# Performance work log

Measured on AMD Instinct MI355X. Metric: run time of the kernel, lower is better.

The kernel has to match this reference:

```python
import jax, jax.numpy as jnp
import numpy as np

ALPHA = 0.2          # LeakyReLU negative slope
NEG_INF = -9e15      # mask value used by the original module


def setup_inputs() -> dict:
    key = jax.random.key(0)
    k1, k2, k3, k4 = jax.random.split(key, 4)
    N, F_IN, F_OUT = 8192, 512, 256
    inp = jax.random.normal(k1, (N, F_IN), dtype=jnp.float32)
    W = jax.random.normal(k2, (F_IN, F_OUT), dtype=jnp.float32) * (1.414 / np.sqrt(F_IN))
    a = jax.random.normal(k3, (2 * F_OUT, 1), dtype=jnp.float32) * (1.414 / np.sqrt(F_OUT))
    adj = jax.random.randint(k4, (N, N), 0, 2, dtype=jnp.int32)
    return {"input": inp, "W": W, "a": a, "adj": adj}


def reference(input, W, a, adj):
    # h: [N, F_out]
    h = input @ W
    F_out = h.shape[1]
    # Original builds a_input[i,j] = concat(h_i, h_j) then matmuls with a.
    # Equivalent: e_ij = leakyrelu(h_i . a[:F] + h_j . a[F:]) without the O(N^2 * 2F) tensor.
    a1 = a[:F_out, 0]   # [F_out]
    a2 = a[F_out:, 0]   # [F_out]
    s1 = h @ a1         # [N]
    s2 = h @ a2         # [N]
    e = jax.nn.leaky_relu(s1[:, None] + s2[None, :], negative_slope=ALPHA)  # [N, N]
    attention = jax.nn.softmax(jnp.where(adj > 0, e, NEG_INF), axis=1)       # [N, N]
    return attention @ h  # [N, F_out]
```

## Files before the change

### kernel.cpp

```cpp
#include <hip/hip_runtime.h>


typedef __attribute__((ext_vector_type(8))) short bf16x8;
typedef __attribute__((ext_vector_type(4))) float fx4;
typedef __attribute__((ext_vector_type(4))) int ix4;
typedef __attribute__((ext_vector_type(2))) unsigned int ux2;

#define NN 8192
#define FIN 512
#define FOUT 256
#define PS 136
#define AROWS 32

__device__ __forceinline__ unsigned short f2bf(float f) {
    unsigned int x = __float_as_uint(f);
    x += 0x7fffu + ((x >> 16) & 1u);
    return (unsigned short)(x >> 16);
}
__device__ __forceinline__ bf16x8 pack8(fx4 a, fx4 b) {
    bf16x8 r;
    r[0] = (short)f2bf(a[0]); r[1] = (short)f2bf(a[1]);
    r[2] = (short)f2bf(a[2]); r[3] = (short)f2bf(a[3]);
    r[4] = (short)f2bf(b[0]); r[5] = (short)f2bf(b[1]);
    r[6] = (short)f2bf(b[2]); r[7] = (short)f2bf(b[3]);
    return r;
}

__global__ void wt_kernel(const float* __restrict__ W,
                          unsigned short* __restrict__ WTt) {
    const int c = threadIdx.x;
    const int k = blockIdx.x;
    WTt[((size_t)(k >> 5) * 256 + c) * 32 + (k & 31)] = f2bf(W[k * FOUT + c]);
}

__global__ __launch_bounds__(256) void prep_kernel(
    const float* __restrict__ X,
    const unsigned short* __restrict__ WTt,
    const float* __restrict__ A,
    const int* __restrict__ adj,
    unsigned short* __restrict__ hTt,
    float* __restrict__ s1, float* __restrict__ s2,
    unsigned int* __restrict__ mask)
{
    __shared__ float s1sh[4][16], s2sh[4][16];
    const int tid = threadIdx.x;

    if (blockIdx.x >= 512) {
        const int g = (blockIdx.x - 512) * 256 + tid;
        const int* base = adj + (size_t)g * 32;
        ix4 v[8];
#pragma unroll
        for (int k = 0; k < 8; ++k) v[k] = *(const ix4*)(base + k * 4);
        unsigned int m = 0;
#pragma unroll
        for (int k = 0; k < 8; ++k)
#pragma unroll
            for (int j = 0; j < 4; ++j)
                m |= (v[k][j] != 0 ? 1u : 0u) << (k * 4 + j);
        mask[g] = m;
        return;
    }

    const int w = tid >> 6, l = tid & 63, q = l >> 4, lr = l & 15;
    const int r0 = blockIdx.x * 16;
    const int cbase = w * 64;
    fx4 acc[4] = {};

    for (int kb = 0; kb < FIN; kb += 32) {
        const float* xp = X + (size_t)(r0 + lr) * FIN + kb + q * 8;
        bf16x8 a0 = pack8(*(const fx4*)xp, *(const fx4*)(xp + 4));
#pragma unroll
        for (int tc = 0; tc < 4; ++tc) {
            bf16x8 b = *(const bf16x8*)(WTt + ((size_t)(kb >> 5) * 256 + cbase + tc * 16 + lr) * 32 + q * 8);
            acc[tc] = __builtin_amdgcn_mfma_f32_16x16x32_bf16(a0, b, acc[tc], 0, 0, 0);
        }
    }

    const int jb = r0 >> 5, jo = (r0 & 31) + q * 4;
#pragma unroll
    for (int tc = 0; tc < 4; ++tc) {
        const int c = cbase + tc * 16 + lr;
        ux2 hp;
        hp.x = (unsigned)f2bf(acc[tc][0]) | ((unsigned)f2bf(acc[tc][1]) << 16);
        hp.y = (unsigned)f2bf(acc[tc][2]) | ((unsigned)f2bf(acc[tc][3]) << 16);
        *(ux2*)(hTt + ((size_t)jb * 256 + c) * 32 + jo) = hp;
    }

    float p1[4] = {}, p2[4] = {};
#pragma unroll
    for (int tc = 0; tc < 4; ++tc) {
        const int c = cbase + tc * 16 + lr;
        const float a1v = A[c], a2v = A[FOUT + c];
#pragma unroll
        for (int r = 0; r < 4; ++r) {
            p1[r] += acc[tc][r] * a1v;
            p2[r] += acc[tc][r] * a2v;
        }
    }
#pragma unroll
    for (int r = 0; r < 4; ++r) {
#pragma unroll
        for (int off = 1; off < 16; off <<= 1) {
            p1[r] += __shfl_xor(p1[r], off);
            p2[r] += __shfl_xor(p2[r], off);
        }
        if (lr == 0) { s1sh[w][q * 4 + r] = p1[r]; s2sh[w][q * 4 + r] = p2[r]; }
    }
    __syncthreads();
    if (tid < 16) {
        s1[r0 + tid] = s1sh[0][tid] + s1sh[1][tid] + s1sh[2][tid] + s1sh[3][tid];
        s2[r0 + tid] = s2sh[0][tid] + s2sh[1][tid] + s2sh[2][tid] + s2sh[3][tid];
    }
}

__global__ __launch_bounds__(512) void attn_kernel(
    const unsigned int* __restrict__ mask,
    const unsigned short* __restrict__ hTt,
    const float* __restrict__ s1,
    const float* __restrict__ s2,
    float* __restrict__ out)
{
    __shared__ unsigned short P[2][AROWS * PS];
    __shared__ float dsh[AROWS];

    const int tid = threadIdx.x;
    const int r0 = blockIdx.x * AROWS;

    const int prow = tid >> 4;
    const int pq = tid & 15;
    const float s1v = s1[r0 + prow];
    const unsigned int* mrow = mask + (size_t)(r0 + prow) * 256;
    const int mshift = (pq & 3) * 8;
    float denp = 0.f;

    const int w = tid >> 6, l = tid & 63, q = l >> 4, lr = l & 15;
    const int cbase = w * 32;
    fx4 acc[2][2] = {};

    struct LSet { unsigned int mval; fx4 s2a, s2b; };
    LSet LA, LB;
    bf16x8 B0[4][2], B1[4][2];

    auto loadP = [&](int kt, LSet& L) {
        L.mval = mrow[kt * 4 + (pq >> 2)];
        L.s2a = *(const fx4*)(s2 + kt * 128 + pq * 8);
        L.s2b = *(const fx4*)(s2 + kt * 128 + pq * 8 + 4);
    };
    auto calcP = [&](int b, const LSet& L) {
        const unsigned int mbyte = (L.mval >> mshift) & 0xFFu;
        bf16x8 pv;
#pragma unroll
        for (int j = 0; j < 8; ++j) {
            const float s2j = (j < 4) ? L.s2a[j] : L.s2b[j - 4];
            float t = s1v + s2j;
            float e = fmaxf(t, 0.2f * t);
            e = fminf(e, 30.f);
            const float p = ((mbyte >> j) & 1u) ? __expf(e) : 0.f;
            denp += p;
            pv[j] = (short)f2bf(p);
        }
        *(bf16x8*)(&P[b][prow * PS + pq * 8]) = pv;
    };
    auto loadB = [&](int it, bf16x8 (&B)[4][2]) {
#pragma unroll
        for (int ks = 0; ks < 4; ++ks)
#pragma unroll
            for (int tc = 0; tc < 2; ++tc)
                B[ks][tc] = *(const bf16x8*)(hTt + ((size_t)(it * 4 + ks) * 256 + cbase + tc * 16 + lr) * 32 + q * 8);
    };

    auto ldsBarrier = [&]() {
        asm volatile("s_waitcnt lgkmcnt(0)" ::: "memory");
        __builtin_amdgcn_s_barrier();
    };

    const int ITERS = NN / 128;
    loadP(0, LA);
    calcP(0, LA);
    loadP(1, LA);
    loadB(0, B0);
    ldsBarrier();

    auto body = [&](int it, bf16x8 (&Bc)[4][2], bf16x8 (&Bn)[4][2],
                    LSet& Lc, LSet& Ln) {
        if (it + 1 < ITERS) loadB(it + 1, Bn);
        if (it + 2 < ITERS) loadP(it + 2, Ln);
        const unsigned short* Pb = P[it & 1];
        bf16x8 af0[4], af1[4];
#pragma unroll
        for (int ks = 0; ks < 4; ++ks) {
            af0[ks] = *(const bf16x8*)(Pb + lr * PS + ks * 32 + q * 8);
            af1[ks] = *(const bf16x8*)(Pb + (16 + lr) * PS + ks * 32 + q * 8);
        }
        __builtin_amdgcn_s_setprio(1);
#pragma unroll
        for (int ks = 0; ks < 4; ++ks)
#pragma unroll
            for (int tc = 0; tc < 2; ++tc) {
                acc[0][tc] = __builtin_amdgcn_mfma_f32_16x16x32_bf16(af0[ks], Bc[ks][tc], acc[0][tc], 0, 0, 0);
                acc[1][tc] = __builtin_amdgcn_mfma_f32_16x16x32_bf16(af1[ks], Bc[ks][tc], acc[1][tc], 0, 0, 0);
            }
        __builtin_amdgcn_s_setprio(0);
        if (it + 1 < ITERS) calcP((it + 1) & 1, Lc);
        ldsBarrier();
    };

    for (int it = 0; it < ITERS; it += 2) {
        body(it, B0, B1, LA, LB);
        body(it + 1, B1, B0, LB, LA);
    }

    float v = denp;
    v += __shfl_xor(v, 1);
    v += __shfl_xor(v, 2);
    v += __shfl_xor(v, 4);
    v += __shfl_xor(v, 8);
    if (pq == 0) dsh[prow] = v;
    __syncthreads();

#pragma unroll
    for (int mg = 0; mg < 2; ++mg) {
#pragma unroll
        for (int r = 0; r < 4; ++r) {
            const int row = mg * 16 + q * 4 + r;
            const float dinv = 1.0f / fmaxf(dsh[row], 1e-30f);
#pragma unroll
            for (int tc = 0; tc < 2; ++tc) {
                out[(size_t)(r0 + row) * FOUT + cbase + tc * 16 + lr] = acc[mg][tc][r] * dinv;
            }
        }
    }
}

extern "C" void kernel_launch(void* const* d_in, const int* in_sizes, int n_in,
                              void* d_out, int out_size, void* d_ws, size_t ws_size,
                              hipStream_t stream) {
    const float *X = nullptr, *W = nullptr, *A = nullptr;
    const int* adj = nullptr;
    for (int i = 0; i < n_in; ++i) {
        switch (in_sizes[i]) {
            case NN * FIN:   X = (const float*)d_in[i]; break;
            case FIN * FOUT: W = (const float*)d_in[i]; break;
            case 2 * FOUT:   A = (const float*)d_in[i]; break;
            case NN * NN:    adj = (const int*)d_in[i]; break;
        }
    }
    if (!X) X = (const float*)d_in[0];
    if (!W) W = (const float*)d_in[1];
    if (!A) A = (const float*)d_in[2];
    if (!adj) adj = (const int*)d_in[3];
    float* out = (float*)d_out;

    char* ws = (char*)d_ws;
    float* s1 = (float*)ws;
    float* s2 = (float*)(ws + 32768);
    unsigned short* WTt = (unsigned short*)(ws + 98304);
    unsigned short* hTt = (unsigned short*)(ws + 360448);
    unsigned int* mask = (unsigned int*)(ws + 5242880);

    wt_kernel<<<512, 256, 0, stream>>>(W, WTt);
    prep_kernel<<<512 + 8192, 256, 0, stream>>>(X, WTt, A, adj, hTt, s1, s2, mask);
    attn_kernel<<<NN / AROWS, 512, 0, stream>>>(mask, hTt, s1, s2, out);
}
```

Measured before the change: 471.7 us.

## Read adjacency directly in attention kernel instead of precomputed bitmask

Removes the bitmask-packing pass from the prep kernel. The attention kernel now streams the int32 adjacency matrix itself with nontemporal loads and tests each entry inline. This saves a separate 256MB read plus an 8MB mask write and re-read. The cost is that the bandwidth-heavy adjacency read moves into the pipelined attention loop, so its latency must be hidden behind the MFMA work there, and registers per thread go up.

```diff
diff --git a/kernel.cpp b/kernel.cpp
--- a/kernel.cpp
+++ b/kernel.cpp
@@ -37,29 +37,11 @@
     const float* __restrict__ X,
     const unsigned short* __restrict__ WTt,
     const float* __restrict__ A,
-    const int* __restrict__ adj,
     unsigned short* __restrict__ hTt,
-    float* __restrict__ s1, float* __restrict__ s2,
-    unsigned int* __restrict__ mask)
+    float* __restrict__ s1, float* __restrict__ s2)
 {
     __shared__ float s1sh[4][16], s2sh[4][16];
     const int tid = threadIdx.x;
-
-    if (blockIdx.x >= 512) {
-        const int g = (blockIdx.x - 512) * 256 + tid;
-        const int* base = adj + (size_t)g * 32;
-        ix4 v[8];
-#pragma unroll
-        for (int k = 0; k < 8; ++k) v[k] = *(const ix4*)(base + k * 4);
-        unsigned int m = 0;
-#pragma unroll
-        for (int k = 0; k < 8; ++k)
-#pragma unroll
-            for (int j = 0; j < 4; ++j)
-                m |= (v[k][j] != 0 ? 1u : 0u) << (k * 4 + j);
-        mask[g] = m;
-        return;
-    }
 
     const int w = tid >> 6, l = tid & 63, q = l >> 4, lr = l & 15;
     const int r0 = blockIdx.x * 16;
@@ -114,7 +96,7 @@
 }
 
 __global__ __launch_bounds__(512) void attn_kernel(
-    const unsigned int* __restrict__ mask,
+    const int* __restrict__ adj,
     const unsigned short* __restrict__ hTt,
     const float* __restrict__ s1,
     const float* __restrict__ s2,
@@ -129,33 +111,34 @@
     const int prow = tid >> 4;
     const int pq = tid & 15;
     const float s1v = s1[r0 + prow];
-    const unsigned int* mrow = mask + (size_t)(r0 + prow) * 256;
-    const int mshift = (pq & 3) * 8;
+    const int* arow = adj + (size_t)(r0 + prow) * NN + pq * 8;
     float denp = 0.f;
 
     const int w = tid >> 6, l = tid & 63, q = l >> 4, lr = l & 15;
     const int cbase = w * 32;
     fx4 acc[2][2] = {};
 
-    struct LSet { unsigned int mval; fx4 s2a, s2b; };
+    struct LSet { ix4 v0, v1; fx4 s2a, s2b; };
     LSet LA, LB;
     bf16x8 B0[4][2], B1[4][2];
 
     auto loadP = [&](int kt, LSet& L) {
-        L.mval = mrow[kt * 4 + (pq >> 2)];
+        const int* ap = arow + kt * 128;
+        L.v0 = __builtin_nontemporal_load((const ix4*)ap);
+        L.v1 = __builtin_nontemporal_load((const ix4*)(ap + 4));
         L.s2a = *(const fx4*)(s2 + kt * 128 + pq * 8);
         L.s2b = *(const fx4*)(s2 + kt * 128 + pq * 8 + 4);
     };
     auto calcP = [&](int b, const LSet& L) {
-        const unsigned int mbyte = (L.mval >> mshift) & 0xFFu;
         bf16x8 pv;
 #pragma unroll
         for (int j = 0; j < 8; ++j) {
+            const int aj = (j < 4) ? L.v0[j] : L.v1[j - 4];
             const float s2j = (j < 4) ? L.s2a[j] : L.s2b[j - 4];
             float t = s1v + s2j;
             float e = fmaxf(t, 0.2f * t);
             e = fminf(e, 30.f);
-            const float p = ((mbyte >> j) & 1u) ? __expf(e) : 0.f;
+            const float p = (aj != 0) ? __expf(e) : 0.f;
             denp += p;
             pv[j] = (short)f2bf(p);
         }
@@ -256,9 +239,8 @@
     float* s2 = (float*)(ws + 32768);
     unsigned short* WTt = (unsigned short*)(ws + 98304);
     unsigned short* hTt = (unsigned short*)(ws + 360448);
-    unsigned int* mask = (unsigned int*)(ws + 5242880);
 
     wt_kernel<<<512, 256, 0, stream>>>(W, WTt);
-    prep_kernel<<<512 + 8192, 256, 0, stream>>>(X, WTt, A, adj, hTt, s1, s2, mask);
-    attn_kernel<<<NN / AROWS, 512, 0, stream>>>(mask, hTt, s1, s2, out);
-}
+    prep_kernel<<<512, 256, 0, stream>>>(X, WTt, A, hTt, s1, s2);
+    attn_kernel<<<NN / AROWS, 512, 0, stream>>>(adj, hTt, s1, s2, out);
+}
```

Result: faster. 442.4 us (-6.2%).
